# Optimization experiments

Measured on AMD Instinct MI355X. Metric: run time of the kernel, lower is better.

## Reference

```python
import jax, jax.numpy as jnp
import numpy as np

B, C, H, W, K, O, KS = 32, 16, 256, 256, 4, 16, 3
C4 = C // 4


def setup_inputs() -> dict:
    key = jax.random.key(0)
    ks = jax.random.split(key, 6)
    return {
        "x": jax.random.normal(ks[0], (B, C, H, W), dtype=jnp.float32),
        "weight": jax.random.normal(ks[1], (K, O, C, KS, KS), dtype=jnp.float32),
        "attn_w1": jax.random.normal(ks[2], (C4, C), dtype=jnp.float32) * 0.1,
        "attn_b1": jnp.zeros((C4,), dtype=jnp.float32),
        "attn_w2": jax.random.normal(ks[3], (K, C4), dtype=jnp.float32) * 0.1,
        "attn_b2": jnp.zeros((K,), dtype=jnp.float32),
    }


def reference(x, weight, attn_w1, attn_b1, attn_w2, attn_b2):
    # Attention branch: global avg pool -> 1x1 conv -> relu -> 1x1 conv -> softmax over K
    pooled = x.mean(axis=(2, 3))                                  # (B, C)
    h = jax.nn.relu(pooled @ attn_w1.T + attn_b1)                 # (B, C//4)
    attn = jax.nn.softmax(h @ attn_w2.T + attn_b2, axis=1)        # (B, K)

    # Per-sample aggregated kernel: sum_k attn[b,k] * weight[k]
    agg_w = jnp.einsum('bk,koihw->boihw', attn, weight)           # (B, O, C, KS, KS)

    # Per-sample conv2d (equivalent to torch grouped conv with groups=B)
    pad = ((1, 1), (1, 1))
    def per_sample(xi, wi):
        # xi: (C, H, W), wi: (O, C, KS, KS)
        return jax.lax.conv_general_dilated(
            xi[None], wi, window_strides=(1, 1), padding=pad,
            dimension_numbers=('NCHW', 'OIHW', 'NCHW'))[0]
    return jax.vmap(per_sample)(x, agg_w)                         # (B, O, H, W)
```

## Files before the change

kernel.cpp:

```cpp
#include <hip/hip_runtime.h>

#define BD  32
#define CD  16
#define HD  256
#define WD  256
#define KD  4
#define OD  16
#define C4D 4

typedef __attribute__((ext_vector_type(8))) short short8v;
typedef __attribute__((ext_vector_type(4))) float float4v;

__device__ float          g_partial[2048];
__device__ unsigned short g_xbf[(size_t)BD * CD * HD * WD];
__device__ unsigned short g_wfrag[BD * 2 * 5 * 64 * 8];

__device__ __forceinline__ unsigned short bf16_rne(float f) {
    unsigned u = __builtin_bit_cast(unsigned, f);
    u += 0x7FFFu + ((u >> 16) & 1u);
    return (unsigned short)(u >> 16);
}
__device__ __forceinline__ float bf16_to_f(unsigned short h) {
    unsigned u = ((unsigned)h) << 16;
    return __builtin_bit_cast(float, u);
}

__global__ void pool_kernel(const float* __restrict__ x) {
    const int plane = blockIdx.x >> 2;
    const int part  = blockIdx.x & 3;
    const size_t base = (size_t)plane * (HD * WD) + part * (HD * WD / 4);
    const float4* xp4 = reinterpret_cast<const float4*>(x + base);

    float4 v[16];
    #pragma unroll
    for (int i = 0; i < 16; ++i) v[i] = xp4[threadIdx.x + i * 256];

    float s = 0.f;
    #pragma unroll
    for (int i = 0; i < 16; ++i) {
        s += (v[i].x + v[i].y) + (v[i].z + v[i].w);
        ushort4 h;
        h.x = bf16_rne(v[i].x); h.y = bf16_rne(v[i].y);
        h.z = bf16_rne(v[i].z); h.w = bf16_rne(v[i].w);
        *reinterpret_cast<ushort4*>(&g_xbf[base + (size_t)(threadIdx.x + i * 256) * 4]) = h;
    }

    __shared__ float red[256];
    red[threadIdx.x] = s;
    __syncthreads();
    for (int off = 128; off > 0; off >>= 1) {
        if (threadIdx.x < off) red[threadIdx.x] += red[threadIdx.x + off];
        __syncthreads();
    }
    if (threadIdx.x == 0) g_partial[blockIdx.x] = red[0];
}

__global__ void attn_agg_kernel(const float* __restrict__ w1, const float* __restrict__ b1,
                                const float* __restrict__ w2, const float* __restrict__ b2,
                                const float* __restrict__ weight) {
    const int b  = blockIdx.x >> 2;
    const int e0 = (blockIdx.x & 3) * 1280;

    float p[CD];
    #pragma unroll
    for (int c = 0; c < CD; ++c) {
        const int i0 = (b * CD + c) * 4;
        p[c] = (g_partial[i0] + g_partial[i0 + 1] + g_partial[i0 + 2] + g_partial[i0 + 3])
               * (1.f / (HD * WD));
    }

    float h[C4D];
    #pragma unroll
    for (int j = 0; j < C4D; ++j) {
        float s = b1[j];
        #pragma unroll
        for (int c = 0; c < CD; ++c) s = fmaf(p[c], w1[j * CD + c], s);
        h[j] = fmaxf(s, 0.f);
    }

    float lg[KD];
    float mx = -1e30f;
    #pragma unroll
    for (int k = 0; k < KD; ++k) {
        float s = b2[k];
        #pragma unroll
        for (int j = 0; j < C4D; ++j) s = fmaf(h[j], w2[k * C4D + j], s);
        lg[k] = s;
        mx = fmaxf(mx, s);
    }
    float se = 0.f;
    #pragma unroll
    for (int k = 0; k < KD; ++k) { lg[k] = expf(lg[k] - mx); se += lg[k]; }
    const float inv = 1.f / se;
    float at[KD];
    #pragma unroll
    for (int k = 0; k < KD; ++k) at[k] = lg[k] * inv;

    for (int e = e0 + threadIdx.x; e < e0 + 1280; e += 256) {
        const int prod = e / 2560;
        const int rem  = e % 2560;
        const int s    = rem / 512;
        const int lr   = rem % 512;
        const int lane = lr >> 3;
        const int i    = lr & 7;
        const int o    = lane & 15;
        const int kg   = lane >> 4;
        const int kk   = kg * 8 + i;
        const int tl   = kk >> 4;
        const int c    = kk & 15;
        const int tap  = 2 * s + tl;
        float v = 0.f;
        if (tap < 9) {
            #pragma unroll
            for (int k = 0; k < KD; ++k)
                v = fmaf(at[k], weight[((k * OD + o) * CD + c) * 9 + tap], v);
        }
        const unsigned short hi = bf16_rne(v);
        unsigned short val = hi;
        if (prod == 1) val = bf16_rne(v - bf16_to_f(hi));
        g_wfrag[b * 5120 + e] = val;
    }
}

__global__ __launch_bounds__(256, 2)
void conv_kernel(float* __restrict__ out) {
    const int b  = blockIdx.y;
    const int tx = blockIdx.x & 3;
    const int ty = blockIdx.x >> 2;
    const int x0 = tx * 64, y0 = ty * 16;

    __shared__ unsigned short xs[18 * 66 * 24];

    for (int grp = threadIdx.x; grp < 288; grp += 256) {
        const int r  = grp >> 4;
        const int j  = grp & 15;
        const int gy = y0 - 1 + r;
        const int gx = x0 + 4 * j;
        const bool ok = (gy >= 0) && (gy < HD);
        uint2 v[16];
        #pragma unroll
        for (int c = 0; c < 16; ++c) {
            v[c] = make_uint2(0u, 0u);
            if (ok)
                v[c] = *reinterpret_cast<const uint2*>(
                    &g_xbf[((size_t)(b * CD + c) * HD + gy) * WD + gx]);
        }
        #pragma unroll
        for (int p = 0; p < 4; ++p) {
            unsigned d[8];
            #pragma unroll
            for (int i = 0; i < 8; ++i) {
                const unsigned a0 = (p < 2) ? v[2 * i].x     : v[2 * i].y;
                const unsigned a1 = (p < 2) ? v[2 * i + 1].x : v[2 * i + 1].y;
                d[i] = (p & 1) ? ((a0 >> 16) | (a1 & 0xFFFF0000u))
                               : ((a0 & 0xFFFFu) | (a1 << 16));
            }
            const int e = r * 66 + 4 * j + 1 + p;
            unsigned* dst = reinterpret_cast<unsigned*>(&xs[e * 24]);
            *reinterpret_cast<uint4*>(dst)     = make_uint4(d[0], d[1], d[2], d[3]);
            *reinterpret_cast<uint4*>(dst + 4) = make_uint4(d[4], d[5], d[6], d[7]);
        }
    }
    if (threadIdx.x < 36) {
        const int r   = threadIdx.x >> 1;
        const int col = (threadIdx.x & 1) ? 65 : 0;
        const int gy  = y0 - 1 + r;
        const int gx  = x0 - 1 + col;
        const bool ok = (gy >= 0) && (gy < HD) && (gx >= 0) && (gx < WD);
        unsigned d[8];
        #pragma unroll
        for (int i = 0; i < 8; ++i) {
            unsigned u0 = 0, u1 = 0;
            if (ok) {
                u0 = g_xbf[((size_t)(b * CD + 2 * i)     * HD + gy) * WD + gx];
                u1 = g_xbf[((size_t)(b * CD + 2 * i + 1) * HD + gy) * WD + gx];
            }
            d[i] = u0 | (u1 << 16);
        }
        const int e = r * 66 + col;
        unsigned* dst = reinterpret_cast<unsigned*>(&xs[e * 24]);
        *reinterpret_cast<uint4*>(dst)     = make_uint4(d[0], d[1], d[2], d[3]);
        *reinterpret_cast<uint4*>(dst + 4) = make_uint4(d[4], d[5], d[6], d[7]);
    }

    const int lane = threadIdx.x & 63;
    const int wv   = threadIdx.x >> 6;

    short8v whi[5], wlo[5];
    {
        const unsigned short* wf = g_wfrag + b * 5120;
        #pragma unroll
        for (int s = 0; s < 5; ++s) {
            whi[s] = *(const short8v*)&wf[s * 512 + lane * 8];
            wlo[s] = *(const short8v*)&wf[2560 + s * 512 + lane * 8];
        }
    }

    const int m     = lane & 15;
    const int kg    = lane >> 4;
    const int tl    = kg >> 1;
    const int chalf = kg & 1;
    int aoff[5];
    #pragma unroll
    for (int s = 0; s < 5; ++s) {
        int tap = 2 * s + tl;
        if (tap > 8) tap = 8;
        const int dy = tap / 3 - 1, dx = tap % 3 - 1;
        aoff[s] = (dy * 66 + dx) * 24;
    }
    const int colbase = 1 + 16 * wv + m;

    __syncthreads();

    #pragma unroll 1
    for (int q2 = 0; q2 < 8; ++q2) {
        const int qa = 2 * q2;
        const int pa = ((qa + 1) * 66 + colbase) * 24 + chalf * 8;
        const int pb = pa + 66 * 24;
        float4v acca = {0.f, 0.f, 0.f, 0.f};
        float4v accb = {0.f, 0.f, 0.f, 0.f};
        #pragma unroll
        for (int s = 0; s < 5; ++s) {
            const short8v Aa = *(const short8v*)&xs[pa + aoff[s]];
            const short8v Ab = *(const short8v*)&xs[pb + aoff[s]];
            acca = __builtin_amdgcn_mfma_f32_16x16x32_bf16(Aa, whi[s], acca, 0, 0, 0);
            accb = __builtin_amdgcn_mfma_f32_16x16x32_bf16(Ab, whi[s], accb, 0, 0, 0);
            acca = __builtin_amdgcn_mfma_f32_16x16x32_bf16(Aa, wlo[s], acca, 0, 0, 0);
            accb = __builtin_amdgcn_mfma_f32_16x16x32_bf16(Ab, wlo[s], accb, 0, 0, 0);
        }
        const int o  = lane & 15;
        const int xc = x0 + 16 * wv + kg * 4;
        float4 va = make_float4(acca[0], acca[1], acca[2], acca[3]);
        float4 vb = make_float4(accb[0], accb[1], accb[2], accb[3]);
        *reinterpret_cast<float4*>(
            &out[((size_t)(b * OD + o) * HD + (y0 + qa)) * WD + xc]) = va;
        *reinterpret_cast<float4*>(
            &out[((size_t)(b * OD + o) * HD + (y0 + qa + 1)) * WD + xc]) = vb;
    }
}

extern "C" void kernel_launch(void* const* d_in, const int* in_sizes, int n_in,
                              void* d_out, int out_size, void* d_ws, size_t ws_size,
                              hipStream_t stream) {
    (void)in_sizes; (void)n_in; (void)out_size; (void)d_ws; (void)ws_size;
    const float* x      = (const float*)d_in[0];
    const float* weight = (const float*)d_in[1];
    const float* w1     = (const float*)d_in[2];
    const float* b1     = (const float*)d_in[3];
    const float* w2     = (const float*)d_in[4];
    const float* b2     = (const float*)d_in[5];
    float* out = (float*)d_out;

    pool_kernel<<<2048, 256, 0, stream>>>(x);
    attn_agg_kernel<<<128, 256, 0, stream>>>(w1, b1, w2, b2, weight);
    conv_kernel<<<dim3(64, 32), 256, 0, stream>>>(out);
}
```

Baseline: 297.5 us.

## Shrink conv tile to 32x16, raise occupancy, stagger LDS staging writes

```diff
diff --git a/kernel.cpp b/kernel.cpp
--- a/kernel.cpp
+++ b/kernel.cpp
@@ -122,18 +122,20 @@
     }
 }
 
-__global__ __launch_bounds__(256, 2)
+__global__ __launch_bounds__(256, 4)
 void conv_kernel(float* __restrict__ out) {
     const int b  = blockIdx.y;
-    const int tx = blockIdx.x & 3;
-    const int ty = blockIdx.x >> 2;
-    const int x0 = tx * 64, y0 = ty * 16;
-
-    __shared__ unsigned short xs[18 * 66 * 24];
-
-    for (int grp = threadIdx.x; grp < 288; grp += 256) {
-        const int r  = grp >> 4;
-        const int j  = grp & 15;
+    const int tx = blockIdx.x & 7;
+    const int ty = blockIdx.x >> 3;
+    const int x0 = tx * 32, y0 = ty * 16;
+
+    __shared__ unsigned short xs[18 * 34 * 24];
+
+    const int tid = threadIdx.x;
+
+    if (tid < 144) {
+        const int r  = tid >> 3;
+        const int j  = tid & 7;
         const int gy = y0 - 1 + r;
         const int gx = x0 + 4 * j;
         const bool ok = (gy >= 0) && (gy < HD);
@@ -147,23 +149,24 @@
         }
         #pragma unroll
         for (int p = 0; p < 4; ++p) {
+            const int pe = (p + j) & 3;
             unsigned d[8];
             #pragma unroll
             for (int i = 0; i < 8; ++i) {
-                const unsigned a0 = (p < 2) ? v[2 * i].x     : v[2 * i].y;
-                const unsigned a1 = (p < 2) ? v[2 * i + 1].x : v[2 * i + 1].y;
-                d[i] = (p & 1) ? ((a0 >> 16) | (a1 & 0xFFFF0000u))
-                               : ((a0 & 0xFFFFu) | (a1 << 16));
+                const unsigned a0 = (pe & 2) ? v[2 * i].y     : v[2 * i].x;
+                const unsigned a1 = (pe & 2) ? v[2 * i + 1].y : v[2 * i + 1].x;
+                d[i] = (pe & 1) ? ((a0 >> 16) | (a1 & 0xFFFF0000u))
+                                : ((a0 & 0xFFFFu) | (a1 << 16));
             }
-            const int e = r * 66 + 4 * j + 1 + p;
+            const int e = r * 34 + 4 * j + 1 + pe;
             unsigned* dst = reinterpret_cast<unsigned*>(&xs[e * 24]);
             *reinterpret_cast<uint4*>(dst)     = make_uint4(d[0], d[1], d[2], d[3]);
             *reinterpret_cast<uint4*>(dst + 4) = make_uint4(d[4], d[5], d[6], d[7]);
         }
-    }
-    if (threadIdx.x < 36) {
-        const int r   = threadIdx.x >> 1;
-        const int col = (threadIdx.x & 1) ? 65 : 0;
+    } else if (tid < 180) {
+        const int t   = tid - 144;
+        const int r   = t >> 1;
+        const int col = (t & 1) ? 33 : 0;
         const int gy  = y0 - 1 + r;
         const int gx  = x0 - 1 + col;
         const bool ok = (gy >= 0) && (gy < HD) && (gx >= 0) && (gx < WD);
@@ -177,7 +180,7 @@
             }
             d[i] = u0 | (u1 << 16);
         }
-        const int e = r * 66 + col;
+        const int e = r * 34 + col;
         unsigned* dst = reinterpret_cast<unsigned*>(&xs[e * 24]);
         *reinterpret_cast<uint4*>(dst)     = make_uint4(d[0], d[1], d[2], d[3]);
         *reinterpret_cast<uint4*>(dst + 4) = make_uint4(d[4], d[5], d[6], d[7]);
@@ -206,17 +209,19 @@
         int tap = 2 * s + tl;
         if (tap > 8) tap = 8;
         const int dy = tap / 3 - 1, dx = tap % 3 - 1;
-        aoff[s] = (dy * 66 + dx) * 24;
-    }
-    const int colbase = 1 + 16 * wv + m;
+        aoff[s] = (dy * 34 + dx) * 24;
+    }
+    const int h       = wv & 1;
+    const int rb      = (wv >> 1) * 8;
+    const int colbase = 1 + 16 * h + m;
 
     __syncthreads();
 
     #pragma unroll 1
-    for (int q2 = 0; q2 < 8; ++q2) {
+    for (int q2 = 0; q2 < 4; ++q2) {
         const int qa = 2 * q2;
-        const int pa = ((qa + 1) * 66 + colbase) * 24 + chalf * 8;
-        const int pb = pa + 66 * 24;
+        const int pa = ((rb + qa + 1) * 34 + colbase) * 24 + chalf * 8;
+        const int pb = pa + 34 * 24;
         float4v acca = {0.f, 0.f, 0.f, 0.f};
         float4v accb = {0.f, 0.f, 0.f, 0.f};
         #pragma unroll
@@ -229,13 +234,14 @@
             accb = __builtin_amdgcn_mfma_f32_16x16x32_bf16(Ab, wlo[s], accb, 0, 0, 0);
         }
         const int o  = lane & 15;
-        const int xc = x0 + 16 * wv + kg * 4;
+        const int xc = x0 + 16 * h + kg * 4;
+        const int y  = y0 + rb + qa;
         float4 va = make_float4(acca[0], acca[1], acca[2], acca[3]);
         float4 vb = make_float4(accb[0], accb[1], accb[2], accb[3]);
         *reinterpret_cast<float4*>(
-            &out[((size_t)(b * OD + o) * HD + (y0 + qa)) * WD + xc]) = va;
+            &out[((size_t)(b * OD + o) * HD + y) * WD + xc]) = va;
         *reinterpret_cast<float4*>(
-            &out[((size_t)(b * OD + o) * HD + (y0 + qa + 1)) * WD + xc]) = vb;
+            &out[((size_t)(b * OD + o) * HD + (y + 1)) * WD + xc]) = vb;
     }
 }
 
@@ -253,5 +259,5 @@
 
     pool_kernel<<<2048, 256, 0, stream>>>(x);
     attn_agg_kernel<<<128, 256, 0, stream>>>(w1, b1, w2, b2, weight);
-    conv_kernel<<<dim3(64, 32), 256, 0, stream>>>(out);
-}
+    conv_kernel<<<dim3(128, 32), 256, 0, stream>>>(out);
+}
```

After: 349.3 us. 17.4% more time.
